# Kernel tuning notes

Measured on AMD Instinct MI355X. Metric: run time of the kernel, lower is better.

Reference implementation:

```python
import jax, jax.numpy as jnp
import numpy as np

D = 128      # memory_dim
L = 64       # segment_len
SCALE = 1.0 / np.sqrt(D)
LN_EPS = 1e-5


def _layernorm(x, g, b):
    mu = x.mean(-1, keepdims=True)
    var = ((x - mu) ** 2).mean(-1, keepdims=True)
    return (x - mu) * jax.lax.rsqrt(var + LN_EPS) * g + b


def setup_inputs() -> dict:
    key = jax.random.key(0)
    ks = jax.random.split(key, 8)
    B, T, Hd = 4, 4096, 2048
    w = 0.02  # init scale for weight matrices
    return {
        "H": jax.random.normal(ks[0], (B, T, Hd), jnp.float32),
        "M": jax.random.normal(ks[1], (B, D, D), jnp.float32),  # [B,K=128,D=128]
        "ln_g": jnp.ones((Hd,), jnp.float32),
        "ln_b": jnp.zeros((Hd,), jnp.float32),
        "W_eta_w": jax.random.normal(ks[2], (Hd,), jnp.float32) * w,
        "W_eta_b": jnp.full((1,), -5.0, jnp.float32),
        "sum_q": jax.random.normal(ks[3], (D,), jnp.float32),
        "sp_w": jax.random.normal(ks[4], (Hd, D), jnp.float32) * w,
        "sp_b": jnp.zeros((D,), jnp.float32),
        "eta_ch": jnp.ones((D,), jnp.float32),
        "temp": jnp.ones((1,), jnp.float32),
        "W_qkv": jax.random.normal(ks[5], (Hd, 3 * D), jnp.float32) * w,
    }


def reference(H, M, ln_g, ln_b, W_eta_w, W_eta_b, sum_q, sp_w, sp_b, eta_ch, temp, W_qkv):
    B, T, _ = H.shape
    K = M.shape[1]
    S = T // L  # T chosen divisible by segment_len (no-pad branch)

    Hn = _layernorm(H, ln_g, ln_b)                      # [B,T,Hd]

    # ---- write_memory ----
    H_mem = Hn @ sp_w + sp_b                            # [B,T,D]
    eta_tokens = jnp.einsum('bth,h->bt', Hn, W_eta_w) + W_eta_b  # [B,T]

    H_segs = H_mem.reshape(B, S, L, D)
    summary_scores = jnp.einsum('d,bsld->bsl', sum_q, H_segs) * SCALE
    summary_w = jax.nn.softmax(summary_scores, axis=-1)
    Z_seg = jnp.einsum('bsl,bsld->bsd', summary_w, H_segs)       # [B,S,D]

    eta_sig = jax.nn.sigmoid(eta_tokens)                          # [B,T]
    eta_seg = eta_sig.reshape(B, S, L).max(axis=-1)[..., None]    # [B,S,1]

    scores = jnp.einsum('bsd,bkd->bsk', Z_seg, M) * SCALE * jnp.exp(temp)
    A = jax.nn.softmax(scores, axis=-1)                           # [B,S,K]
    DeltaM = jnp.einsum('bsk,bsd->bkd', A, Z_seg * eta_seg)       # [B,K,D]

    eta_avg = eta_seg.mean(axis=1, keepdims=True)                 # [B,1,1]
    gate = eta_avg * jax.nn.sigmoid(eta_ch)                       # [B,1,D]
    M_new = (1.0 - gate) * M + DeltaM / S

    norm_sq = jnp.sum(DeltaM ** 2) / S
    # diversity loss on M_new
    Mn = M_new / jnp.maximum(jnp.linalg.norm(M_new, axis=-1, keepdims=True), 1e-12)
    sim = jnp.einsum('bkd,bjd->bkj', Mn, Mn) * (1.0 - jnp.eye(K, dtype=M.dtype))
    div_loss = jnp.mean(sim ** 2)
    loss = norm_sq * 0.01 + div_loss * 0.1

    # ---- read_memory (from updated memory; K<=1024 -> dense softmax path) ----
    Q_r = Hn @ W_qkv[:, 2 * D:]                                   # [B,T,D]
    r_scores = jnp.einsum('btd,bkd->btk', Q_r, M_new)
    A_r = jax.nn.softmax(r_scores * 2.0, axis=-1)
    C = jnp.einsum('btk,bkd->btd', A_r, M_new)                    # [B,T,D]

    return C, loss
```

## Files before the change

kernel.cpp:

```cpp
#include <hip/hip_runtime.h>
#include <hip/hip_bf16.h>
#include <math.h>

#define HD   2048
#define DD   128
#define TT   4096
#define BB   4
#define MT   (BB*TT)
#define LSEG 64
#define SSEG 64
#define NCOL 256
#define SCALE_D 0.088388347648318447f

typedef _Float16 half8 __attribute__((ext_vector_type(8)));
typedef _Float16 half4v __attribute__((ext_vector_type(4)));
typedef float    f32x4 __attribute__((ext_vector_type(4)));

__device__ __forceinline__ float sigmf(float x){ return 1.f/(1.f+__expf(-x)); }

__device__ __forceinline__ void glds16(const void* g, void* l) {
  __builtin_amdgcn_global_load_lds(
      (const __attribute__((address_space(1))) unsigned int*)g,
      (__attribute__((address_space(3))) unsigned int*)l, 16, 0, 0);
}

__global__ void k_pre(const float* __restrict__ ln_g, const float* __restrict__ ln_b,
                      const float* __restrict__ sp_w, const float* __restrict__ sp_b,
                      const float* __restrict__ W_qkv, const float* __restrict__ W_eta_w,
                      const float* __restrict__ W_eta_b,
                      _Float16* __restrict__ Bp, float* __restrict__ s_vec,
                      float* __restrict__ cb_vec, float* __restrict__ we2,
                      float* __restrict__ scal)
{
  __shared__ float red1[256], red2[256];
  int n = blockIdx.x, t = threadIdx.x;
  float sp = 0.f, cp = 0.f;
  if (n < NCOL) {
    for (int h = t; h < HD; h += 256) {
      float w = (n < DD) ? sp_w[(size_t)h*DD + n] : W_qkv[(size_t)h*384 + 256 + (n-DD)];
      float g = ln_g[h], b = ln_b[h];
      Bp[(size_t)n*HD + h] = (_Float16)(g*w);
      sp += g*w; cp += b*w;
    }
  } else {
    for (int h = t; h < HD; h += 256) {
      float w = W_eta_w[h];
      float g = ln_g[h], b = ln_b[h];
      we2[h] = g*w;
      sp += g*w; cp += b*w;
    }
  }
  red1[t] = sp; red2[t] = cp;
  __syncthreads();
  for (int o = 128; o > 0; o >>= 1) {
    if (t < o) { red1[t] += red1[t+o]; red2[t] += red2[t+o]; }
    __syncthreads();
  }
  if (t == 0) {
    if (n < NCOL) {
      s_vec[n]  = red1[0];
      cb_vec[n] = red2[0] + ((n < DD) ? sp_b[n] : 0.f);
    } else {
      scal[0] = red1[0];
      scal[1] = red2[0] + W_eta_b[0];
      scal[2] = 0.f; scal[3] = 0.f;
    }
  }
}

__launch_bounds__(512, 2)
__global__ void k01(const float* __restrict__ H, const _Float16* __restrict__ Bp,
                    const float* __restrict__ s_vec, const float* __restrict__ cb_vec,
                    const float* __restrict__ we2, const float* __restrict__ scal,
                    const float* __restrict__ sum_q, const float* __restrict__ Mmat,
                    const float* __restrict__ temp,
                    float* __restrict__ Q_r, float* __restrict__ Zeta,
                    float* __restrict__ A_seg, float* __restrict__ eta_seg)
{
  __shared__ __align__(16) char pool[114688];
  __shared__ float we_s[HD];
  __shared__ float smu[64], srs[64], seta[64];
  __shared__ float sq_s[128], w64_s[64], Zs[128], red_s[4];
  __shared__ float eta_sh_s;
  _Float16* sA  = (_Float16*)pool;
  _Float16* sB  = (_Float16*)(pool + 16384);
  float*    sHm = (float*)pool;

  int tid = threadIdx.x;
  int seg = blockIdx.x;
  int b   = seg >> 6;
  int m0  = seg * 64;
  int w = tid >> 6, lane = tid & 63;
  int wr = w >> 2, wc = w & 3;
  int fcol = lane & 15, kq = lane >> 4;

  for (int i = tid; i < HD/4; i += 512)
    ((float4*)we_s)[i] = ((const float4*)we2)[i];
  if (tid < 128) sq_s[tid] = sum_q[tid];
  float scal0 = scal[0], scal1 = scal[1];
  __syncthreads();

  int r_l = tid >> 3, s8 = tid & 7;
  const float* aptr = H + (size_t)(m0 + r_l)*HD + s8*8;
  int bn[4], bsl[4];
#pragma unroll
  for (int i = 0; i < 4; ++i) {
    int idx = i*512 + tid;
    bn[i]  = idx >> 3;
    bsl[i] = (idx & 7) ^ (bn[i] & 7);
  }

  f32x4 acc[2][4];
#pragma unroll
  for (int i = 0; i < 2; ++i)
#pragma unroll
    for (int j = 0; j < 4; ++j) acc[i][j] = (f32x4){0.f,0.f,0.f,0.f};
  float s1 = 0.f, s2 = 0.f, se = 0.f;

  float4 paE0 = *(const float4*)(aptr + 0);
  float4 paE1 = *(const float4*)(aptr + 4);
#pragma unroll
  for (int i = 0; i < 4; ++i)
    glds16(Bp + (size_t)bn[i]*HD + bsl[i]*8, sB + (size_t)(i*512 + tid)*8);
  float4 paO0 = *(const float4*)(aptr + 64);
  float4 paO1 = *(const float4*)(aptr + 68);
#pragma unroll
  for (int i = 0; i < 4; ++i)
    glds16(Bp + (size_t)bn[i]*HD + 64 + bsl[i]*8,
           sB + 16384 + (size_t)(i*512 + tid)*8);

  int cur3 = 0;

#define KSTEP(KT, P0, P1, VMASM, PREFETCH, BISSUE)                            \
  {                                                                           \
    _Float16* sAc = sA + ((KT)&1)*4096;                                       \
    _Float16* sBc = sB + cur3*16384;                                          \
    int k0 = (KT)*64;                                                         \
    float v[8] = {P0.x,P0.y,P0.z,P0.w, P1.x,P1.y,P1.z,P1.w};                  \
    if (PREFETCH) {                                                           \
      const float* ap_ = aptr + ((KT)+2)*64;                                  \
      P0 = *(const float4*)(ap_ + 0);                                         \
      P1 = *(const float4*)(ap_ + 4);                                         \
    }                                                                         \
    {                                                                         \
      const float4* wv4 = (const float4*)(we_s + k0 + s8*8);                  \
      float4 u0 = wv4[0], u1 = wv4[1];                                        \
      float uu[8] = {u0.x,u0.y,u0.z,u0.w, u1.x,u1.y,u1.z,u1.w};               \
      half8 h0;                                                               \
      _Pragma("unroll")                                                       \
      for (int j = 0; j < 8; ++j) {                                           \
        s1 += v[j]; s2 += v[j]*v[j]; se += v[j]*uu[j];                        \
        h0[j] = (_Float16)v[j];                                               \
      }                                                                       \
      *(half8*)&sAc[r_l*64 + (s8 ^ (r_l & 7))*8] = h0;                        \
    }                                                                         \
    asm volatile(VMASM ::: "memory");                                         \
    __builtin_amdgcn_s_barrier();                                             \
    __builtin_amdgcn_sched_barrier(0);                                        \
    if (BISSUE) {                                                             \
      int wb3 = cur3 + 2; if (wb3 >= 3) wb3 -= 3;                             \
      _Float16* sBn = sB + wb3*16384;                                         \
      const _Float16* bsrc = Bp + (k0 + 128);                                 \
      _Pragma("unroll")                                                       \
      for (int i = 0; i < 4; ++i)                                             \
        glds16(bsrc + (size_t)bn[i]*HD + bsl[i]*8,                            \
               sBn + (size_t)(i*512 + tid)*8);                                \
      __builtin_amdgcn_sched_barrier(0);                                      \
    }                                                                         \
    __builtin_amdgcn_s_setprio(1);                                            \
    _Pragma("unroll")                                                         \
    for (int ks = 0; ks < 2; ++ks) {                                          \
      half8 af[2], bf[4];                                                     \
      _Pragma("unroll")                                                       \
      for (int rt = 0; rt < 2; ++rt) {                                        \
        int r = wr*32 + rt*16 + fcol;                                         \
        int ch = (ks*4 + kq) ^ (r & 7);                                       \
        af[rt] = *(half8*)&sAc[r*64 + ch*8];                                  \
      }                                                                       \
      _Pragma("unroll")                                                       \
      for (int ct = 0; ct < 4; ++ct) {                                        \
        int n = wc*64 + ct*16 + fcol;                                         \
        int ch = (ks*4 + kq) ^ (n & 7);                                       \
        bf[ct] = *(half8*)&sBc[n*64 + ch*8];                                  \
      }                                                                       \
      _Pragma("unroll")                                                       \
      for (int rt = 0; rt < 2; ++rt)                                          \
        _Pragma("unroll")                                                     \
        for (int ct = 0; ct < 4; ++ct)                                        \
          acc[rt][ct] = __builtin_amdgcn_mfma_f32_16x16x32_f16(af[rt], bf[ct], acc[rt][ct], 0,0,0); \
    }                                                                         \
    __builtin_amdgcn_s_setprio(0);                                            \
    cur3 += 1; if (cur3 >= 3) cur3 -= 3;                                      \
  }

#pragma unroll 1
  for (int kp = 0; kp < 15; ++kp) {
    KSTEP(2*kp,   paE0, paE1, "s_waitcnt vmcnt(8) lgkmcnt(0)", 1, 1)
    KSTEP(2*kp+1, paO0, paO1, "s_waitcnt vmcnt(8) lgkmcnt(0)", 1, 1)
  }
  KSTEP(30, paE0, paE1, "s_waitcnt vmcnt(6) lgkmcnt(0)", 0, 0)
  KSTEP(31, paO0, paO1, "s_waitcnt vmcnt(0) lgkmcnt(0)", 0, 0)
#undef KSTEP

  s1 += __shfl_xor(s1, 1); s1 += __shfl_xor(s1, 2); s1 += __shfl_xor(s1, 4);
  s2 += __shfl_xor(s2, 1); s2 += __shfl_xor(s2, 2); s2 += __shfl_xor(s2, 4);
  se += __shfl_xor(se, 1); se += __shfl_xor(se, 2); se += __shfl_xor(se, 4);
  if (s8 == 0) {
    float mu   = s1 * (1.f/HD);
    float var  = s2 * (1.f/HD) - mu*mu;
    float rstd = rsqrtf(var + 1e-5f);
    smu[r_l] = mu; srs[r_l] = rstd;
    seta[r_l] = rstd*(se - mu*scal0) + scal1;
  }
  __syncthreads();

#pragma unroll
  for (int ct = 0; ct < 4; ++ct) {
    int nl = wc*64 + ct*16 + fcol;
    float sn = s_vec[nl], cbn = cb_vec[nl];
#pragma unroll
    for (int rt = 0; rt < 2; ++rt)
#pragma unroll
      for (int r = 0; r < 4; ++r) {
        int m = wr*32 + rt*16 + kq*4 + r;
        sHm[m*260 + nl] = srs[m]*(acc[rt][ct][r] - smu[m]*sn) + cbn;
      }
  }
  __syncthreads();

#pragma unroll
  for (int j = 0; j < 4; ++j) {
    int idx = j*512 + tid;
    int row = idx >> 5, c4 = (idx & 31)*4;
    *(float4*)&Q_r[(size_t)(m0 + row)*DD + c4] = *(float4*)&sHm[row*260 + 128 + c4];
  }

  if (w == 0) {
    float sc = 0.f;
    const float4* hrow = (const float4*)&sHm[lane*260];
#pragma unroll
    for (int d4 = 0; d4 < 32; ++d4) {
      float4 hv = hrow[d4];
      float4 qv = *(const float4*)&sq_s[d4*4];
      sc += hv.x*qv.x + hv.y*qv.y + hv.z*qv.z + hv.w*qv.w;
    }
    sc *= SCALE_D;
    float mx = sc;
    for (int o = 32; o > 0; o >>= 1) mx = fmaxf(mx, __shfl_xor(mx, o));
    float e = __expf(sc - mx);
    float sm = e;
    for (int o = 32; o > 0; o >>= 1) sm += __shfl_xor(sm, o);
    w64_s[lane] = e / sm;
  } else if (w == 1) {
    float ev = seta[lane];
    for (int o = 32; o > 0; o >>= 1) ev = fmaxf(ev, __shfl_xor(ev, o));
    if (lane == 0) { float es = sigmf(ev); eta_sh_s = es; eta_seg[seg] = es; }
  }
  __syncthreads();

  if (tid < 128) {
    float z = 0.f;
    for (int l = 0; l < 64; ++l) z += w64_s[l]*sHm[l*260 + tid];
    Zs[tid] = z;
    Zeta[(size_t)seg*DD + tid] = z * eta_sh_s;
  }
  __syncthreads();

  float sc2 = 0.f;
  if (tid < 128) {
    const float4* mrow = (const float4*)(Mmat + ((size_t)b*DD + tid)*DD);
#pragma unroll
    for (int d4 = 0; d4 < 32; ++d4) {
      float4 mv = mrow[d4];
      sc2 += mv.x*Zs[d4*4] + mv.y*Zs[d4*4+1] + mv.z*Zs[d4*4+2] + mv.w*Zs[d4*4+3];
    }
    sc2 *= SCALE_D * __expf(temp[0]);
    float mx = sc2;
    for (int o = 32; o > 0; o >>= 1) mx = fmaxf(mx, __shfl_xor(mx, o));
    if (lane == 0) red_s[w] = mx;
  }
  __syncthreads();
  float ev2 = 0.f;
  if (tid < 128) {
    float mx = fmaxf(red_s[0], red_s[1]);
    ev2 = __expf(sc2 - mx);
    float sm = ev2;
    for (int o = 32; o > 0; o >>= 1) sm += __shfl_xor(sm, o);
    if (lane == 0) red_s[2 + w] = sm;
  }
  __syncthreads();
  if (tid < 128) {
    float smt = red_s[2] + red_s[3];
    A_seg[(size_t)seg*DD + tid] = ev2 / smt;
  }
}

__global__ void k2b(const float* __restrict__ A_seg, const float* __restrict__ Zeta,
                    const float* __restrict__ eta_seg, const float* __restrict__ Mmat,
                    const float* __restrict__ eta_ch,
                    float* __restrict__ M_new, float* __restrict__ rns_arr,
                    float* __restrict__ scal)
{
  __shared__ float As[64][33];
  __shared__ __align__(16) float Zsl[64*128];
  __shared__ float rowp[32][8];
  __shared__ float eta_av;
  __shared__ float redb[4];
  int tid = threadIdx.x;
  int b = blockIdx.x >> 2, kq = blockIdx.x & 3;
  for (int i = tid; i < 64*32; i += 256) {
    int s = i >> 5, j = i & 31;
    As[s][j] = A_seg[((size_t)b*SSEG + s)*DD + kq*32 + j];
  }
  const float4* z4 = (const float4*)(Zeta + (size_t)b*SSEG*DD);
  float4* zs4 = (float4*)Zsl;
  for (int i = tid; i < 64*32; i += 256) zs4[i] = z4[i];
  if (tid < 64) {
    float ev = eta_seg[(size_t)b*SSEG + tid];
    for (int o=32;o>0;o>>=1) ev += __shfl_xor(ev, o);
    if (tid == 0) eta_av = ev * (1.f/SSEG);
  }
  __syncthreads();
  int kl = tid & 31, dg = tid >> 5;
  int k = kq*32 + kl, d0 = dg*16;
  float dm[16];
#pragma unroll
  for (int j=0;j<16;j++) dm[j]=0.f;
  for (int s = 0; s < 64; ++s) {
    float a = As[s][kl];
    const float* zr = &Zsl[s*128 + d0];
#pragma unroll
    for (int j=0;j<16;j++) dm[j] += a * zr[j];
  }
  float nsq = 0.f;
#pragma unroll
  for (int j=0;j<16;j++) nsq += dm[j]*dm[j];
  float eav = eta_av;
  float mn[16];
  float ss = 0.f;
#pragma unroll
  for (int j=0;j<16;j++) {
    int d = d0 + j;
    float gate = eav * sigmf(eta_ch[d]);
    float v = (1.f - gate)*Mmat[((size_t)b*DD + k)*DD + d] + dm[j]*(1.f/SSEG);
    mn[j] = v; ss += v*v;
  }
#pragma unroll
  for (int j=0;j<16;j+=4) {
    float4 v4; v4.x=mn[j]; v4.y=mn[j+1]; v4.z=mn[j+2]; v4.w=mn[j+3];
    *(float4*)&M_new[((size_t)b*DD + k)*DD + d0 + j] = v4;
  }
  rowp[kl][dg] = ss;
  for (int o=1;o<64;o<<=1) nsq += __shfl_xor(nsq, o);
  if ((tid&63)==0) redb[tid>>6] = nsq;
  __syncthreads();
  if (tid == 0) atomicAdd(&scal[2], redb[0]+redb[1]+redb[2]+redb[3]);
  if (tid < 32) {
    float t2 = 0.f;
#pragma unroll
    for (int g=0; g<8; ++g) t2 += rowp[tid][g];
    float nrm = sqrtf(t2);
    rns_arr[(size_t)b*DD + kq*32 + tid] = 1.f / fmaxf(nrm, 1e-12f);
  }
}

__global__ void k2d(const float* __restrict__ M_new, const float* __restrict__ rns_arr,
                    float* __restrict__ scal)
{
  __shared__ float kr[4][128];
  __shared__ float redb[4];
  int tid = threadIdx.x;
  int b = blockIdx.x >> 5, kq = blockIdx.x & 31;
  for (int i = tid; i < 4*128; i += 256) {
    int ki = i >> 7, d = i & 127;
    kr[ki][d] = M_new[((size_t)b*DD + kq*4 + ki)*DD + d];
  }
  __syncthreads();
  int j = tid & 127, kh = tid >> 7;
  const float* mj = &M_new[((size_t)b*DD + j)*DD];
  float rj = rns_arr[(size_t)b*DD + j];
  float dv = 0.f;
#pragma unroll
  for (int ki2 = 0; ki2 < 2; ++ki2) {
    int kil = kh*2 + ki2;
    int kk = kq*4 + kil;
    float dot = 0.f;
    for (int d = 0; d < 128; d += 4) {
      float4 a = *(const float4*)(mj + d);
      dot += a.x*kr[kil][d] + a.y*kr[kil][d+1] + a.z*kr[kil][d+2] + a.w*kr[kil][d+3];
    }
    if (kk != j) {
      float sv = dot * rj * rns_arr[(size_t)b*DD + kk];
      dv += sv*sv;
    }
  }
  for (int o=1;o<64;o<<=1) dv += __shfl_xor(dv, o);
  if ((tid&63)==0) redb[tid>>6] = dv;
  __syncthreads();
  if (tid==0) atomicAdd(&scal[3], redb[0]+redb[1]+redb[2]+redb[3]);
}

__launch_bounds__(256, 1)
__global__ void k3(const float* __restrict__ Q_r, const float* __restrict__ M_new,
                   const float* __restrict__ scal, float* __restrict__ out)
{
  __shared__ __align__(16) _Float16 Mq[128*132];
  __shared__ __align__(16) _Float16 Mt[128*136];
  __shared__ __align__(16) _Float16 Ps[64*132];
  int tid = threadIdx.x;
  int b = blockIdx.x >> 6, tile = blockIdx.x & 63;
  int t0 = tile*64;
  if (blockIdx.x == 0 && tid == 0) {
    float loss = 0.01f*(scal[2]*(1.f/SSEG)) + 0.1f*(scal[3]*(1.f/(BB*DD*DD)));
    out[(size_t)MT*DD] = loss;
  }
  const float4* m4 = (const float4*)(M_new + (size_t)b*DD*DD);
#pragma unroll
  for (int it = 0; it < 4; ++it) {
    int sb = it*256 + tid;
    int rb = sb & 31, cb = sb >> 5;
    int r0 = rb*4, c0 = cb*4;
    float a[4][4];
#pragma unroll
    for (int j = 0; j < 4; ++j) {
      float4 v = m4[(size_t)(r0+j)*32 + cb];
      a[j][0]=v.x; a[j][1]=v.y; a[j][2]=v.z; a[j][3]=v.w;
    }
#pragma unroll
    for (int j = 0; j < 4; ++j) {
      half4v h; h.x=(_Float16)a[j][0]; h.y=(_Float16)a[j][1];
                h.z=(_Float16)a[j][2]; h.w=(_Float16)a[j][3];
      *(half4v*)&Mq[(r0+j)*132 + c0] = h;
    }
#pragma unroll
    for (int j2 = 0; j2 < 4; ++j2) {
      half4v h; h.x=(_Float16)a[0][j2]; h.y=(_Float16)a[1][j2];
                h.z=(_Float16)a[2][j2]; h.w=(_Float16)a[3][j2];
      *(half4v*)&Mt[(c0+j2)*136 + r0] = h;
    }
  }
  int w = tid >> 6, lane = tid & 63;
  int fcol = lane & 15, kq = lane >> 4;
  int tokA = t0 + w*16 + fcol;
  size_t qbase = ((size_t)b*TT + tokA)*DD;
  half8 af[4];
#pragma unroll
  for (int ks = 0; ks < 4; ++ks) {
    float4 q0 = *(const float4*)&Q_r[qbase + ks*32 + kq*8];
    float4 q1 = *(const float4*)&Q_r[qbase + ks*32 + kq*8 + 4];
    half8 h;
    h[0]=(_Float16)q0.x; h[1]=(_Float16)q0.y; h[2]=(_Float16)q0.z; h[3]=(_Float16)q0.w;
    h[4]=(_Float16)q1.x; h[5]=(_Float16)q1.y; h[6]=(_Float16)q1.z; h[7]=(_Float16)q1.w;
    af[ks] = h;
  }
  __syncthreads();
  f32x4 sacc[8];
#pragma unroll
  for (int nt = 0; nt < 8; ++nt) sacc[nt] = (f32x4){0.f,0.f,0.f,0.f};
#pragma unroll
  for (int nt = 0; nt < 8; ++nt)
#pragma unroll
    for (int ks = 0; ks < 4; ++ks) {
      half8 bf = *(half8*)&Mq[(nt*16 + fcol)*132 + ks*32 + kq*8];
      sacc[nt] = __builtin_amdgcn_mfma_f32_16x16x32_f16(af[ks], bf, sacc[nt], 0,0,0);
    }
#pragma unroll
  for (int nt = 0; nt < 8; ++nt)
#pragma unroll
    for (int r = 0; r < 4; ++r) sacc[nt][r] *= 2.f;
  float mx[4], sm[4];
#pragma unroll
  for (int r = 0; r < 4; ++r) {
    float m = sacc[0][r];
#pragma unroll
    for (int nt = 1; nt < 8; ++nt) m = fmaxf(m, sacc[nt][r]);
#pragma unroll
    for (int o = 1; o < 16; o <<= 1) m = fmaxf(m, __shfl_xor(m, o));
    mx[r] = m;
  }
#pragma unroll
  for (int r = 0; r < 4; ++r) sm[r] = 0.f;
#pragma unroll
  for (int nt = 0; nt < 8; ++nt)
#pragma unroll
    for (int r = 0; r < 4; ++r) {
      float e = __expf(sacc[nt][r] - mx[r]);
      sacc[nt][r] = e; sm[r] += e;
    }
#pragma unroll
  for (int r = 0; r < 4; ++r) {
    float s = sm[r];
#pragma unroll
    for (int o = 1; o < 16; o <<= 1) s += __shfl_xor(s, o);
    sm[r] = 1.f / s;
  }
#pragma unroll
  for (int nt = 0; nt < 8; ++nt)
#pragma unroll
    for (int r = 0; r < 4; ++r) {
      int tk = w*16 + kq*4 + r;
      Ps[tk*132 + nt*16 + fcol] = (_Float16)(sacc[nt][r]*sm[r]);
    }
  __syncthreads();
  half8 pf[4];
#pragma unroll
  for (int ks = 0; ks < 4; ++ks)
    pf[ks] = *(half8*)&Ps[(w*16 + fcol)*132 + ks*32 + kq*8];
  f32x4 cacc[8];
#pragma unroll
  for (int nt = 0; nt < 8; ++nt) cacc[nt] = (f32x4){0.f,0.f,0.f,0.f};
#pragma unroll
  for (int nt = 0; nt < 8; ++nt)
#pragma unroll
    for (int ks = 0; ks < 4; ++ks) {
      half8 bf = *(half8*)&Mt[(nt*16 + fcol)*136 + ks*32 + kq*8];
      cacc[nt] = __builtin_amdgcn_mfma_f32_16x16x32_f16(pf[ks], bf, cacc[nt], 0,0,0);
    }
#pragma unroll
  for (int nt = 0; nt < 8; ++nt)
#pragma unroll
    for (int r = 0; r < 4; ++r) {
      int tk = t0 + w*16 + kq*4 + r;
      out[((size_t)b*TT + tk)*DD + nt*16 + fcol] = cacc[nt][r];
    }
}

extern "C" void kernel_launch(void* const* d_in, const int* in_sizes, int n_in,
                              void* d_out, int out_size, void* d_ws, size_t ws_size,
                              hipStream_t stream)
{
  (void)in_sizes; (void)n_in; (void)out_size; (void)ws_size;
  const float* H       = (const float*)d_in[0];
  const float* Mmat    = (const float*)d_in[1];
  const float* ln_g    = (const float*)d_in[2];
  const float* ln_b    = (const float*)d_in[3];
  const float* W_eta_w = (const float*)d_in[4];
  const float* W_eta_b = (const float*)d_in[5];
  const float* sum_q   = (const float*)d_in[6];
  const float* sp_w    = (const float*)d_in[7];
  const float* sp_b    = (const float*)d_in[8];
  const float* eta_ch  = (const float*)d_in[9];
  const float* temp    = (const float*)d_in[10];
  const float* W_qkv   = (const float*)d_in[11];
  float* out           = (float*)d_out;

  char* wsb = (char*)d_ws;
  size_t off = 0;
  auto alloc = [&](size_t bytes) -> void* {
    void* p = wsb + off;
    off = (off + bytes + 255) & ~(size_t)255;
    return p;
  };
  _Float16* Bp   = (_Float16*)alloc((size_t)NCOL*HD*2);
  float* s_vec   = (float*)alloc(NCOL*4);
  float* cb_vec  = (float*)alloc(NCOL*4);
  float* we2     = (float*)alloc(HD*4);
  float* scal    = (float*)alloc(4*4);
  float* Q_r     = (float*)alloc((size_t)MT*DD*4);
  float* Zeta    = (float*)alloc((size_t)BB*SSEG*DD*4);
  float* A_seg   = (float*)alloc((size_t)BB*SSEG*DD*4);
  float* eta_seg = (float*)alloc((size_t)BB*SSEG*4);
  float* M_new   = (float*)alloc((size_t)BB*DD*DD*4);
  float* rns_arr = (float*)alloc((size_t)BB*DD*4);

  hipLaunchKernelGGL(k_pre, dim3(NCOL+1), dim3(256), 0, stream,
                     ln_g, ln_b, sp_w, sp_b, W_qkv, W_eta_w, W_eta_b,
                     Bp, s_vec, cb_vec, we2, scal);
  hipLaunchKernelGGL(k01, dim3(MT/64), dim3(512), 0, stream,
                     H, Bp, s_vec, cb_vec, we2, scal, sum_q, Mmat, temp,
                     Q_r, Zeta, A_seg, eta_seg);
  hipLaunchKernelGGL(k2b, dim3(16), dim3(256), 0, stream,
                     A_seg, Zeta, eta_seg, Mmat, eta_ch, M_new, rns_arr, scal);
  hipLaunchKernelGGL(k2d, dim3(128), dim3(256), 0, stream,
                     M_new, rns_arr, scal);
  hipLaunchKernelGGL(k3, dim3(256), dim3(256), 0, stream,
                     Q_r, M_new, scal, out);
}
```

Baseline: 87.06 us.

## Deepen k01 GEMM pipeline to four B stages and four-step A prefetch

Changes the fused layernorm+GEMM kernel's main loop from a 3-stage LDS ring for B with 2-step-ahead register prefetch of H to a 4-stage B ring with 4-step-ahead H prefetch. The loop is unrolled by four with static buffer indices, and the vmcnt waits are retuned. The goal is to hide more global-memory latency on the H stream and the weight tiles. In exchange it uses more LDS (pool grows to 144KB) and more registers, which may reduce occupancy below the 2 blocks per CU the launch bounds target.

```diff
diff --git a/kernel.cpp b/kernel.cpp
--- a/kernel.cpp
+++ b/kernel.cpp
@@ -77,7 +77,7 @@
                     float* __restrict__ Q_r, float* __restrict__ Zeta,
                     float* __restrict__ A_seg, float* __restrict__ eta_seg)
 {
-  __shared__ __align__(16) char pool[114688];
+  __shared__ __align__(16) char pool[147456];
   __shared__ float we_s[HD];
   __shared__ float smu[64], srs[64], seta[64];
   __shared__ float sq_s[128], w64_s[64], Zs[128], red_s[4];
@@ -117,32 +117,35 @@
     for (int j = 0; j < 4; ++j) acc[i][j] = (f32x4){0.f,0.f,0.f,0.f};
   float s1 = 0.f, s2 = 0.f, se = 0.f;
 
-  float4 paE0 = *(const float4*)(aptr + 0);
-  float4 paE1 = *(const float4*)(aptr + 4);
+  float4 q0a = *(const float4*)(aptr + 0),   q0b = *(const float4*)(aptr + 4);
+  float4 q1a = *(const float4*)(aptr + 64),  q1b = *(const float4*)(aptr + 68);
+  __builtin_amdgcn_sched_barrier(0);
 #pragma unroll
   for (int i = 0; i < 4; ++i)
     glds16(Bp + (size_t)bn[i]*HD + bsl[i]*8, sB + (size_t)(i*512 + tid)*8);
-  float4 paO0 = *(const float4*)(aptr + 64);
-  float4 paO1 = *(const float4*)(aptr + 68);
+  __builtin_amdgcn_sched_barrier(0);
+  float4 q2a = *(const float4*)(aptr + 128), q2b = *(const float4*)(aptr + 132);
+  __builtin_amdgcn_sched_barrier(0);
 #pragma unroll
   for (int i = 0; i < 4; ++i)
     glds16(Bp + (size_t)bn[i]*HD + 64 + bsl[i]*8,
            sB + 16384 + (size_t)(i*512 + tid)*8);
-
-  int cur3 = 0;
-
-#define KSTEP(KT, P0, P1, VMASM, PREFETCH, BISSUE)                            \
+  __builtin_amdgcn_sched_barrier(0);
+  float4 q3a = *(const float4*)(aptr + 192), q3b = *(const float4*)(aptr + 196);
+  __builtin_amdgcn_sched_barrier(0);
+#pragma unroll
+  for (int i = 0; i < 4; ++i)
+    glds16(Bp + (size_t)bn[i]*HD + 128 + bsl[i]*8,
+           sB + 32768 + (size_t)(i*512 + tid)*8);
+  __builtin_amdgcn_sched_barrier(0);
+
+#define KSTEP(K0V, SAB, SBBUF, SBNB, P0, P1, VMASM, APREF, BISSUE)            \
   {                                                                           \
-    _Float16* sAc = sA + ((KT)&1)*4096;                                       \
-    _Float16* sBc = sB + cur3*16384;                                          \
-    int k0 = (KT)*64;                                                         \
-    float v[8] = {P0.x,P0.y,P0.z,P0.w, P1.x,P1.y,P1.z,P1.w};                  \
-    if (PREFETCH) {                                                           \
-      const float* ap_ = aptr + ((KT)+2)*64;                                  \
-      P0 = *(const float4*)(ap_ + 0);                                         \
-      P1 = *(const float4*)(ap_ + 4);                                         \
-    }                                                                         \
+    _Float16* sAc = sA + (SAB)*4096;                                          \
+    _Float16* sBc = sB + (SBBUF)*16384;                                       \
+    const int k0 = (K0V);                                                     \
     {                                                                         \
+      float v[8] = {P0.x,P0.y,P0.z,P0.w, P1.x,P1.y,P1.z,P1.w};                \
       const float4* wv4 = (const float4*)(we_s + k0 + s8*8);                  \
       float4 u0 = wv4[0], u1 = wv4[1];                                        \
       float uu[8] = {u0.x,u0.y,u0.z,u0.w, u1.x,u1.y,u1.z,u1.w};               \
@@ -158,13 +161,18 @@
     __builtin_amdgcn_s_barrier();                                             \
     __builtin_amdgcn_sched_barrier(0);                                        \
     if (BISSUE) {                                                             \
-      int wb3 = cur3 + 2; if (wb3 >= 3) wb3 -= 3;                             \
-      _Float16* sBn = sB + wb3*16384;                                         \
-      const _Float16* bsrc = Bp + (k0 + 128);                                 \
+      _Float16* sBn = sB + (SBNB)*16384;                                      \
+      const _Float16* bsrc = Bp + (k0 + 192);                                 \
       _Pragma("unroll")                                                       \
       for (int i = 0; i < 4; ++i)                                             \
         glds16(bsrc + (size_t)bn[i]*HD + bsl[i]*8,                            \
                sBn + (size_t)(i*512 + tid)*8);                                \
+      __builtin_amdgcn_sched_barrier(0);                                      \
+    }                                                                         \
+    if (APREF) {                                                              \
+      const float* ap_ = aptr + k0 + 256;                                     \
+      P0 = *(const float4*)(ap_ + 0);                                         \
+      P1 = *(const float4*)(ap_ + 4);                                         \
       __builtin_amdgcn_sched_barrier(0);                                      \
     }                                                                         \
     __builtin_amdgcn_s_setprio(1);                                            \
@@ -190,16 +198,24 @@
           acc[rt][ct] = __builtin_amdgcn_mfma_f32_16x16x32_f16(af[rt], bf[ct], acc[rt][ct], 0,0,0); \
     }                                                                         \
     __builtin_amdgcn_s_setprio(0);                                            \
-    cur3 += 1; if (cur3 >= 3) cur3 -= 3;                                      \
-  }
-
+  }
+
+  KSTEP(0,   0, 0, 3, q0a, q0b, "s_waitcnt vmcnt(12) lgkmcnt(0)", 1, 1)
+  KSTEP(64,  1, 1, 0, q1a, q1b, "s_waitcnt vmcnt(12) lgkmcnt(0)", 1, 1)
+  KSTEP(128, 0, 2, 1, q2a, q2b, "s_waitcnt vmcnt(12) lgkmcnt(0)", 1, 1)
+  KSTEP(192, 1, 3, 2, q3a, q3b, "s_waitcnt vmcnt(14) lgkmcnt(0)", 1, 1)
 #pragma unroll 1
-  for (int kp = 0; kp < 15; ++kp) {
-    KSTEP(2*kp,   paE0, paE1, "s_waitcnt vmcnt(8) lgkmcnt(0)", 1, 1)
-    KSTEP(2*kp+1, paO0, paO1, "s_waitcnt vmcnt(8) lgkmcnt(0)", 1, 1)
-  }
-  KSTEP(30, paE0, paE1, "s_waitcnt vmcnt(6) lgkmcnt(0)", 0, 0)
-  KSTEP(31, paO0, paO1, "s_waitcnt vmcnt(0) lgkmcnt(0)", 0, 0)
+  for (int kp = 1; kp < 7; ++kp) {
+    int j0 = kp*256;
+    KSTEP(j0,     0, 0, 3, q0a, q0b, "s_waitcnt vmcnt(14) lgkmcnt(0)", 1, 1)
+    KSTEP(j0+64,  1, 1, 0, q1a, q1b, "s_waitcnt vmcnt(14) lgkmcnt(0)", 1, 1)
+    KSTEP(j0+128, 0, 2, 1, q2a, q2b, "s_waitcnt vmcnt(14) lgkmcnt(0)", 1, 1)
+    KSTEP(j0+192, 1, 3, 2, q3a, q3b, "s_waitcnt vmcnt(14) lgkmcnt(0)", 1, 1)
+  }
+  KSTEP(1792, 0, 0, 3, q0a, q0b, "s_waitcnt vmcnt(14) lgkmcnt(0)", 0, 1)
+  KSTEP(1856, 1, 1, 0, q1a, q1b, "s_waitcnt vmcnt(12) lgkmcnt(0)", 0, 0)
+  KSTEP(1920, 0, 2, 1, q2a, q2b, "s_waitcnt vmcnt(6) lgkmcnt(0)",  0, 0)
+  KSTEP(1984, 1, 3, 2, q3a, q3b, "s_waitcnt vmcnt(0) lgkmcnt(0)",  0, 0)
 #undef KSTEP
 
   s1 += __shfl_xor(s1, 1); s1 += __shfl_xor(s1, 2); s1 += __shfl_xor(s1, 4);
```

New measurement: 89.00 us. 1.02x slower.

## Halve K-tile of fused LN-GEMM kernel to fit four blocks per CU

Applied to the files above, without the earlier changes.

Shrinks the fused LayerNorm+projection kernel's K-step from 64 to 32 and cuts the LDS pool from about 114KB to 65KB, moving we_s into the pool. Launch bounds rise to 4 blocks per SM so more waves can hide the H loads and the B-panel global_load_lds traffic. The pipeline gets a new swizzle and tuned waitcnt values, and the loop now runs 64 steps with twice as many barriers. sHm epilogue reuse of the smaller pool (64 rows by 260 floats is about 66.5KB) must still fit, and the register cap tightens.

```diff
diff --git a/kernel.cpp b/kernel.cpp
--- a/kernel.cpp
+++ b/kernel.cpp
@@ -68,7 +68,7 @@
   }
 }
 
-__launch_bounds__(512, 2)
+__launch_bounds__(512, 4)
 __global__ void k01(const float* __restrict__ H, const _Float16* __restrict__ Bp,
                     const float* __restrict__ s_vec, const float* __restrict__ cb_vec,
                     const float* __restrict__ we2, const float* __restrict__ scal,
@@ -77,14 +77,14 @@
                     float* __restrict__ Q_r, float* __restrict__ Zeta,
                     float* __restrict__ A_seg, float* __restrict__ eta_seg)
 {
-  __shared__ __align__(16) char pool[114688];
-  __shared__ float we_s[HD];
+  __shared__ __align__(16) char pool[66560];
   __shared__ float smu[64], srs[64], seta[64];
   __shared__ float sq_s[128], w64_s[64], Zs[128], red_s[4];
   __shared__ float eta_sh_s;
-  _Float16* sA  = (_Float16*)pool;
-  _Float16* sB  = (_Float16*)(pool + 16384);
-  float*    sHm = (float*)pool;
+  _Float16* sA   = (_Float16*)pool;
+  _Float16* sB   = (_Float16*)(pool + 8192);
+  float*    we_s = (float*)(pool + 57344);
+  float*    sHm  = (float*)pool;
 
   int tid = threadIdx.x;
   int seg = blockIdx.x;
@@ -94,20 +94,18 @@
   int wr = w >> 2, wc = w & 3;
   int fcol = lane & 15, kq = lane >> 4;
 
-  for (int i = tid; i < HD/4; i += 512)
-    ((float4*)we_s)[i] = ((const float4*)we2)[i];
+  ((float4*)we_s)[tid] = ((const float4*)we2)[tid];
   if (tid < 128) sq_s[tid] = sum_q[tid];
-  float scal0 = scal[0], scal1 = scal[1];
-  __syncthreads();
-
-  int r_l = tid >> 3, s8 = tid & 7;
-  const float* aptr = H + (size_t)(m0 + r_l)*HD + s8*8;
-  int bn[4], bsl[4];
-#pragma unroll
-  for (int i = 0; i < 4; ++i) {
+  __syncthreads();
+
+  int r_l = tid >> 3, s4 = tid & 7;
+  const float* aptr = H + (size_t)(m0 + r_l)*HD + s4*4;
+  int bn[2], bsl[2];
+#pragma unroll
+  for (int i = 0; i < 2; ++i) {
     int idx = i*512 + tid;
-    bn[i]  = idx >> 3;
-    bsl[i] = (idx & 7) ^ (bn[i] & 7);
+    bn[i]  = idx >> 2;
+    bsl[i] = (idx & 3) ^ ((bn[i] >> 1) & 3);
   }
 
   f32x4 acc[2][4];
@@ -117,71 +115,61 @@
     for (int j = 0; j < 4; ++j) acc[i][j] = (f32x4){0.f,0.f,0.f,0.f};
   float s1 = 0.f, s2 = 0.f, se = 0.f;
 
-  float4 paE0 = *(const float4*)(aptr + 0);
-  float4 paE1 = *(const float4*)(aptr + 4);
-#pragma unroll
-  for (int i = 0; i < 4; ++i)
-    glds16(Bp + (size_t)bn[i]*HD + bsl[i]*8, sB + (size_t)(i*512 + tid)*8);
-  float4 paO0 = *(const float4*)(aptr + 64);
-  float4 paO1 = *(const float4*)(aptr + 68);
-#pragma unroll
-  for (int i = 0; i < 4; ++i)
-    glds16(Bp + (size_t)bn[i]*HD + 64 + bsl[i]*8,
-           sB + 16384 + (size_t)(i*512 + tid)*8);
+  float4 paE = *(const float4*)(aptr);
+  __builtin_amdgcn_sched_barrier(0);
+  glds16(Bp + (size_t)bn[0]*HD + bsl[0]*8, sB + (size_t)tid*8);
+  glds16(Bp + (size_t)bn[1]*HD + bsl[1]*8, sB + (size_t)(512 + tid)*8);
+  __builtin_amdgcn_sched_barrier(0);
+  float4 paO = *(const float4*)(aptr + 32);
+  __builtin_amdgcn_sched_barrier(0);
+  glds16(Bp + (size_t)bn[0]*HD + 32 + bsl[0]*8, sB + 8192 + (size_t)tid*8);
+  glds16(Bp + (size_t)bn[1]*HD + 32 + bsl[1]*8, sB + 8192 + (size_t)(512 + tid)*8);
+  __builtin_amdgcn_sched_barrier(0);
 
   int cur3 = 0;
 
-#define KSTEP(KT, P0, P1, VMASM, PREFETCH, BISSUE)                            \
+#define KSTEP(K0V, SAB, P, VMASM, APREF, BISSUE)                              \
   {                                                                           \
-    _Float16* sAc = sA + ((KT)&1)*4096;                                       \
-    _Float16* sBc = sB + cur3*16384;                                          \
-    int k0 = (KT)*64;                                                         \
-    float v[8] = {P0.x,P0.y,P0.z,P0.w, P1.x,P1.y,P1.z,P1.w};                  \
-    if (PREFETCH) {                                                           \
-      const float* ap_ = aptr + ((KT)+2)*64;                                  \
-      P0 = *(const float4*)(ap_ + 0);                                         \
-      P1 = *(const float4*)(ap_ + 4);                                         \
-    }                                                                         \
+    _Float16* sAc = sA + (SAB)*2048;                                          \
+    _Float16* sBc = sB + cur3*8192;                                           \
+    const int k0 = (K0V);                                                     \
     {                                                                         \
-      const float4* wv4 = (const float4*)(we_s + k0 + s8*8);                  \
-      float4 u0 = wv4[0], u1 = wv4[1];                                        \
-      float uu[8] = {u0.x,u0.y,u0.z,u0.w, u1.x,u1.y,u1.z,u1.w};               \
-      half8 h0;                                                               \
-      _Pragma("unroll")                                                       \
-      for (int j = 0; j < 8; ++j) {                                           \
-        s1 += v[j]; s2 += v[j]*v[j]; se += v[j]*uu[j];                        \
-        h0[j] = (_Float16)v[j];                                               \
-      }                                                                       \
-      *(half8*)&sAc[r_l*64 + (s8 ^ (r_l & 7))*8] = h0;                        \
+      float v0 = P.x, v1 = P.y, v2 = P.z, v3 = P.w;                           \
+      const float4 u = *(const float4*)(we_s + k0 + s4*4);                    \
+      s1 += (v0+v1)+(v2+v3);                                                  \
+      s2 += (v0*v0+v1*v1)+(v2*v2+v3*v3);                                      \
+      se += (v0*u.x+v1*u.y)+(v2*u.z+v3*u.w);                                  \
+      half4v h; h.x=(_Float16)v0; h.y=(_Float16)v1;                           \
+                h.z=(_Float16)v2; h.w=(_Float16)v3;                           \
+      *(half4v*)&sAc[r_l*32 + (((s4>>1)^((r_l>>1)&3))<<3) + ((s4&1)<<2)] = h; \
     }                                                                         \
     asm volatile(VMASM ::: "memory");                                         \
     __builtin_amdgcn_s_barrier();                                             \
     __builtin_amdgcn_sched_barrier(0);                                        \
     if (BISSUE) {                                                             \
       int wb3 = cur3 + 2; if (wb3 >= 3) wb3 -= 3;                             \
-      _Float16* sBn = sB + wb3*16384;                                         \
-      const _Float16* bsrc = Bp + (k0 + 128);                                 \
-      _Pragma("unroll")                                                       \
-      for (int i = 0; i < 4; ++i)                                             \
-        glds16(bsrc + (size_t)bn[i]*HD + bsl[i]*8,                            \
-               sBn + (size_t)(i*512 + tid)*8);                                \
+      _Float16* sBn = sB + wb3*8192;                                          \
+      const _Float16* bsrc = Bp + (k0 + 64);                                  \
+      glds16(bsrc + (size_t)bn[0]*HD + bsl[0]*8, sBn + (size_t)tid*8);        \
+      glds16(bsrc + (size_t)bn[1]*HD + bsl[1]*8, sBn + (size_t)(512+tid)*8);  \
+      __builtin_amdgcn_sched_barrier(0);                                      \
+    }                                                                         \
+    if (APREF) {                                                              \
+      P = *(const float4*)(aptr + k0 + 64);                                   \
       __builtin_amdgcn_sched_barrier(0);                                      \
     }                                                                         \
     __builtin_amdgcn_s_setprio(1);                                            \
-    _Pragma("unroll")                                                         \
-    for (int ks = 0; ks < 2; ++ks) {                                          \
+    {                                                                         \
       half8 af[2], bf[4];                                                     \
       _Pragma("unroll")                                                       \
       for (int rt = 0; rt < 2; ++rt) {                                        \
         int r = wr*32 + rt*16 + fcol;                                         \
-        int ch = (ks*4 + kq) ^ (r & 7);                                       \
-        af[rt] = *(half8*)&sAc[r*64 + ch*8];                                  \
+        af[rt] = *(half8*)&sAc[r*32 + ((kq ^ ((r>>1)&3))<<3)];                \
       }                                                                       \
       _Pragma("unroll")                                                       \
       for (int ct = 0; ct < 4; ++ct) {                                        \
         int n = wc*64 + ct*16 + fcol;                                         \
-        int ch = (ks*4 + kq) ^ (n & 7);                                       \
-        bf[ct] = *(half8*)&sBc[n*64 + ch*8];                                  \
+        bf[ct] = *(half8*)&sBc[n*32 + ((kq ^ ((n>>1)&3))<<3)];                \
       }                                                                       \
       _Pragma("unroll")                                                       \
       for (int rt = 0; rt < 2; ++rt)                                          \
@@ -194,18 +182,20 @@
   }
 
 #pragma unroll 1
-  for (int kp = 0; kp < 15; ++kp) {
-    KSTEP(2*kp,   paE0, paE1, "s_waitcnt vmcnt(8) lgkmcnt(0)", 1, 1)
-    KSTEP(2*kp+1, paO0, paO1, "s_waitcnt vmcnt(8) lgkmcnt(0)", 1, 1)
-  }
-  KSTEP(30, paE0, paE1, "s_waitcnt vmcnt(6) lgkmcnt(0)", 0, 0)
-  KSTEP(31, paO0, paO1, "s_waitcnt vmcnt(0) lgkmcnt(0)", 0, 0)
+  for (int kp = 0; kp < 31; ++kp) {
+    int j0 = kp*64;
+    KSTEP(j0,      0, paE, "s_waitcnt vmcnt(3) lgkmcnt(0)", 1, 1)
+    KSTEP(j0 + 32, 1, paO, "s_waitcnt vmcnt(3) lgkmcnt(0)", 1, 1)
+  }
+  KSTEP(1984, 0, paE, "s_waitcnt vmcnt(3) lgkmcnt(0)", 0, 0)
+  KSTEP(2016, 1, paO, "s_waitcnt vmcnt(0) lgkmcnt(0)", 0, 0)
 #undef KSTEP
 
   s1 += __shfl_xor(s1, 1); s1 += __shfl_xor(s1, 2); s1 += __shfl_xor(s1, 4);
   s2 += __shfl_xor(s2, 1); s2 += __shfl_xor(s2, 2); s2 += __shfl_xor(s2, 4);
   se += __shfl_xor(se, 1); se += __shfl_xor(se, 2); se += __shfl_xor(se, 4);
-  if (s8 == 0) {
+  float scal0 = scal[0], scal1 = scal[1];
+  if (s4 == 0) {
     float mu   = s1 * (1.f/HD);
     float var  = s2 * (1.f/HD) - mu*mu;
     float rstd = rsqrtf(var + 1e-5f);
```

New measurement: 107.8 us. 1.24x slower.

## Load H A-fragments directly into registers, dropping the LDS staging for A

Applied to the files above, without the earlier changes.

Each wave now loads the fp32 H rows it needs for its MFMA A-fragments straight from global memory into registers and converts them to fp16 in place. This removes the LDS A buffer, its writes and reads, and shrinks shared memory. The layernorm and eta statistics are computed only by two waves that between them cover all rows, and the loop is unrolled so the triple B buffer indices are compile-time constants. The cost is that every wave re-reads overlapping H rows from global memory (each row is loaded by four waves), and register pressure rises from holding sixteen float4 prefetch values.

```diff
diff --git a/kernel.cpp b/kernel.cpp
--- a/kernel.cpp
+++ b/kernel.cpp
@@ -22,6 +22,20 @@
   __builtin_amdgcn_global_load_lds(
       (const __attribute__((address_space(1))) unsigned int*)g,
       (__attribute__((address_space(3))) unsigned int*)l, 16, 0, 0);
+}
+
+__device__ __forceinline__ half8 cvt8(float4 a, float4 b) {
+  half8 h;
+  h[0]=(_Float16)a.x; h[1]=(_Float16)a.y; h[2]=(_Float16)a.z; h[3]=(_Float16)a.w;
+  h[4]=(_Float16)b.x; h[5]=(_Float16)b.y; h[6]=(_Float16)b.z; h[7]=(_Float16)b.w;
+  return h;
+}
+
+__device__ __forceinline__ void acc3(float4 v, float4 u,
+                                     float& s1, float& s2, float& se) {
+  s1 += (v.x+v.y)+(v.z+v.w);
+  s2 += (v.x*v.x+v.y*v.y)+(v.z*v.z+v.w*v.w);
+  se += (v.x*u.x+v.y*u.y)+(v.z*u.z+v.w*u.w);
 }
 
 __global__ void k_pre(const float* __restrict__ ln_g, const float* __restrict__ ln_b,
@@ -77,13 +91,12 @@
                     float* __restrict__ Q_r, float* __restrict__ Zeta,
                     float* __restrict__ A_seg, float* __restrict__ eta_seg)
 {
-  __shared__ __align__(16) char pool[114688];
+  __shared__ __align__(16) char pool[98304];
   __shared__ float we_s[HD];
   __shared__ float smu[64], srs[64], seta[64];
   __shared__ float sq_s[128], w64_s[64], Zs[128], red_s[4];
   __shared__ float eta_sh_s;
-  _Float16* sA  = (_Float16*)pool;
-  _Float16* sB  = (_Float16*)(pool + 16384);
+  _Float16* sB  = (_Float16*)pool;
   float*    sHm = (float*)pool;
 
   int tid = threadIdx.x;
@@ -93,6 +106,7 @@
   int w = tid >> 6, lane = tid & 63;
   int wr = w >> 2, wc = w & 3;
   int fcol = lane & 15, kq = lane >> 4;
+  bool SW = (w == 0) || (w == 7);
 
   for (int i = tid; i < HD/4; i += 512)
     ((float4*)we_s)[i] = ((const float4*)we2)[i];
@@ -100,8 +114,9 @@
   float scal0 = scal[0], scal1 = scal[1];
   __syncthreads();
 
-  int r_l = tid >> 3, s8 = tid & 7;
-  const float* aptr = H + (size_t)(m0 + r_l)*HD + s8*8;
+  int ra = m0 + wr*32 + fcol, rb = ra + 16;
+  const float* aA = H + (size_t)ra*HD + kq*8;
+  const float* aB = H + (size_t)rb*HD + kq*8;
   int bn[4], bsl[4];
 #pragma unroll
   for (int i = 0; i < 4; ++i) {
@@ -115,51 +130,55 @@
   for (int i = 0; i < 2; ++i)
 #pragma unroll
     for (int j = 0; j < 4; ++j) acc[i][j] = (f32x4){0.f,0.f,0.f,0.f};
-  float s1 = 0.f, s2 = 0.f, se = 0.f;
-
-  float4 paE0 = *(const float4*)(aptr + 0);
-  float4 paE1 = *(const float4*)(aptr + 4);
+  float s1a=0.f,s2a=0.f,sea=0.f, s1b=0.f,s2b=0.f,seb=0.f;
+
+  float4 E0,E1,E2,E3,E4,E5,E6,E7, O0,O1,O2,O3,O4,O5,O6,O7;
+  E0=*(const float4*)(aA+0);  E1=*(const float4*)(aA+4);
+  E2=*(const float4*)(aA+32); E3=*(const float4*)(aA+36);
+  E4=*(const float4*)(aB+0);  E5=*(const float4*)(aB+4);
+  E6=*(const float4*)(aB+32); E7=*(const float4*)(aB+36);
+  __builtin_amdgcn_sched_barrier(0);
 #pragma unroll
   for (int i = 0; i < 4; ++i)
     glds16(Bp + (size_t)bn[i]*HD + bsl[i]*8, sB + (size_t)(i*512 + tid)*8);
-  float4 paO0 = *(const float4*)(aptr + 64);
-  float4 paO1 = *(const float4*)(aptr + 68);
+  __builtin_amdgcn_sched_barrier(0);
+  O0=*(const float4*)(aA+64); O1=*(const float4*)(aA+68);
+  O2=*(const float4*)(aA+96); O3=*(const float4*)(aA+100);
+  O4=*(const float4*)(aB+64); O5=*(const float4*)(aB+68);
+  O6=*(const float4*)(aB+96); O7=*(const float4*)(aB+100);
+  __builtin_amdgcn_sched_barrier(0);
 #pragma unroll
   for (int i = 0; i < 4; ++i)
     glds16(Bp + (size_t)bn[i]*HD + 64 + bsl[i]*8,
            sB + 16384 + (size_t)(i*512 + tid)*8);
-
-  int cur3 = 0;
-
-#define KSTEP(KT, P0, P1, VMASM, PREFETCH, BISSUE)                            \
+  __builtin_amdgcn_sched_barrier(0);
+
+#define KSTEP(K0V, CUR, WB, P0,P1,P2,P3,P4,P5,P6,P7, VMASM, ISSUE)            \
   {                                                                           \
-    _Float16* sAc = sA + ((KT)&1)*4096;                                       \
-    _Float16* sBc = sB + cur3*16384;                                          \
-    int k0 = (KT)*64;                                                         \
-    float v[8] = {P0.x,P0.y,P0.z,P0.w, P1.x,P1.y,P1.z,P1.w};                  \
-    if (PREFETCH) {                                                           \
-      const float* ap_ = aptr + ((KT)+2)*64;                                  \
-      P0 = *(const float4*)(ap_ + 0);                                         \
-      P1 = *(const float4*)(ap_ + 4);                                         \
+    _Float16* sBc = sB + (CUR)*16384;                                         \
+    const int k0 = (K0V);                                                     \
+    if (SW) {                                                                 \
+      float4 u0 = *(const float4*)(we_s + k0 + kq*8);                         \
+      float4 u1 = *(const float4*)(we_s + k0 + kq*8 + 4);                     \
+      float4 u2 = *(const float4*)(we_s + k0 + 32 + kq*8);                    \
+      float4 u3 = *(const float4*)(we_s + k0 + 32 + kq*8 + 4);                \
+      acc3(P0,u0,s1a,s2a,sea); acc3(P1,u1,s1a,s2a,sea);                       \
+      acc3(P2,u2,s1a,s2a,sea); acc3(P3,u3,s1a,s2a,sea);                       \
+      acc3(P4,u0,s1b,s2b,seb); acc3(P5,u1,s1b,s2b,seb);                       \
+      acc3(P6,u2,s1b,s2b,seb); acc3(P7,u3,s1b,s2b,seb);                       \
     }                                                                         \
-    {                                                                         \
-      const float4* wv4 = (const float4*)(we_s + k0 + s8*8);                  \
-      float4 u0 = wv4[0], u1 = wv4[1];                                        \
-      float uu[8] = {u0.x,u0.y,u0.z,u0.w, u1.x,u1.y,u1.z,u1.w};               \
-      half8 h0;                                                               \
-      _Pragma("unroll")                                                       \
-      for (int j = 0; j < 8; ++j) {                                           \
-        s1 += v[j]; s2 += v[j]*v[j]; se += v[j]*uu[j];                        \
-        h0[j] = (_Float16)v[j];                                               \
-      }                                                                       \
-      *(half8*)&sAc[r_l*64 + (s8 ^ (r_l & 7))*8] = h0;                        \
-    }                                                                         \
+    half8 afA0 = cvt8(P0,P1), afA1 = cvt8(P2,P3);                             \
+    half8 afB0 = cvt8(P4,P5), afB1 = cvt8(P6,P7);                             \
     asm volatile(VMASM ::: "memory");                                         \
     __builtin_amdgcn_s_barrier();                                             \
     __builtin_amdgcn_sched_barrier(0);                                        \
-    if (BISSUE) {                                                             \
-      int wb3 = cur3 + 2; if (wb3 >= 3) wb3 -= 3;                             \
-      _Float16* sBn = sB + wb3*16384;                                         \
+    if (ISSUE) {                                                              \
+      P0=*(const float4*)(aA+k0+128); P1=*(const float4*)(aA+k0+132);         \
+      P2=*(const float4*)(aA+k0+160); P3=*(const float4*)(aA+k0+164);         \
+      P4=*(const float4*)(aB+k0+128); P5=*(const float4*)(aB+k0+132);         \
+      P6=*(const float4*)(aB+k0+160); P7=*(const float4*)(aB+k0+164);         \
+      __builtin_amdgcn_sched_barrier(0);                                      \
+      _Float16* sBn = sB + (WB)*16384;                                        \
       const _Float16* bsrc = Bp + (k0 + 128);                                 \
       _Pragma("unroll")                                                       \
       for (int i = 0; i < 4; ++i)                                             \
@@ -170,47 +189,58 @@
     __builtin_amdgcn_s_setprio(1);                                            \
     _Pragma("unroll")                                                         \
     for (int ks = 0; ks < 2; ++ks) {                                          \
-      half8 af[2], bf[4];                                                     \
-      _Pragma("unroll")                                                       \
-      for (int rt = 0; rt < 2; ++rt) {                                        \
-        int r = wr*32 + rt*16 + fcol;                                         \
-        int ch = (ks*4 + kq) ^ (r & 7);                                       \
-        af[rt] = *(half8*)&sAc[r*64 + ch*8];                                  \
-      }                                                                       \
+      half8 bf[4];                                                            \
       _Pragma("unroll")                                                       \
       for (int ct = 0; ct < 4; ++ct) {                                        \
         int n = wc*64 + ct*16 + fcol;                                         \
         int ch = (ks*4 + kq) ^ (n & 7);                                       \
         bf[ct] = *(half8*)&sBc[n*64 + ch*8];                                  \
       }                                                                       \
+      half8 a0 = ks ? afA1 : afA0;                                            \
+      half8 a1 = ks ? afB1 : afB0;                                            \
       _Pragma("unroll")                                                       \
-      for (int rt = 0; rt < 2; ++rt)                                          \
-        _Pragma("unroll")                                                     \
-        for (int ct = 0; ct < 4; ++ct)                                        \
-          acc[rt][ct] = __builtin_amdgcn_mfma_f32_16x16x32_f16(af[rt], bf[ct], acc[rt][ct], 0,0,0); \
+      for (int ct = 0; ct < 4; ++ct) {                                        \
+        acc[0][ct] = __builtin_amdgcn_mfma_f32_16x16x32_f16(a0, bf[ct], acc[0][ct], 0,0,0); \
+        acc[1][ct] = __builtin_amdgcn_mfma_f32_16x16x32_f16(a1, bf[ct], acc[1][ct], 0,0,0); \
+      }                                                                       \
     }                                                                         \
     __builtin_amdgcn_s_setprio(0);                                            \
-    cur3 += 1; if (cur3 >= 3) cur3 -= 3;                                      \
   }
 
 #pragma unroll 1
-  for (int kp = 0; kp < 15; ++kp) {
-    KSTEP(2*kp,   paE0, paE1, "s_waitcnt vmcnt(8) lgkmcnt(0)", 1, 1)
-    KSTEP(2*kp+1, paO0, paO1, "s_waitcnt vmcnt(8) lgkmcnt(0)", 1, 1)
-  }
-  KSTEP(30, paE0, paE1, "s_waitcnt vmcnt(6) lgkmcnt(0)", 0, 0)
-  KSTEP(31, paO0, paO1, "s_waitcnt vmcnt(0) lgkmcnt(0)", 0, 0)
+  for (int kp = 0; kp < 5; ++kp) {
+    int j0 = kp*384;
+    KSTEP(j0,       0, 2, E0,E1,E2,E3,E4,E5,E6,E7, "s_waitcnt vmcnt(12)", 1)
+    KSTEP(j0 + 64,  1, 0, O0,O1,O2,O3,O4,O5,O6,O7, "s_waitcnt vmcnt(12)", 1)
+    KSTEP(j0 + 128, 2, 1, E0,E1,E2,E3,E4,E5,E6,E7, "s_waitcnt vmcnt(12)", 1)
+    KSTEP(j0 + 192, 0, 2, O0,O1,O2,O3,O4,O5,O6,O7, "s_waitcnt vmcnt(12)", 1)
+    KSTEP(j0 + 256, 1, 0, E0,E1,E2,E3,E4,E5,E6,E7, "s_waitcnt vmcnt(12)", 1)
+    KSTEP(j0 + 320, 2, 1, O0,O1,O2,O3,O4,O5,O6,O7, "s_waitcnt vmcnt(12)", 1)
+  }
+  KSTEP(1920, 0, 2, E0,E1,E2,E3,E4,E5,E6,E7, "s_waitcnt vmcnt(12)", 0)
+  KSTEP(1984, 1, 0, O0,O1,O2,O3,O4,O5,O6,O7, "s_waitcnt vmcnt(0)",  0)
 #undef KSTEP
 
-  s1 += __shfl_xor(s1, 1); s1 += __shfl_xor(s1, 2); s1 += __shfl_xor(s1, 4);
-  s2 += __shfl_xor(s2, 1); s2 += __shfl_xor(s2, 2); s2 += __shfl_xor(s2, 4);
-  se += __shfl_xor(se, 1); se += __shfl_xor(se, 2); se += __shfl_xor(se, 4);
-  if (s8 == 0) {
-    float mu   = s1 * (1.f/HD);
-    float var  = s2 * (1.f/HD) - mu*mu;
-    float rstd = rsqrtf(var + 1e-5f);
-    smu[r_l] = mu; srs[r_l] = rstd;
-    seta[r_l] = rstd*(se - mu*scal0) + scal1;
+  if (SW) {
+    s1a += __shfl_xor(s1a,16); s1a += __shfl_xor(s1a,32);
+    s2a += __shfl_xor(s2a,16); s2a += __shfl_xor(s2a,32);
+    sea += __shfl_xor(sea,16); sea += __shfl_xor(sea,32);
+    s1b += __shfl_xor(s1b,16); s1b += __shfl_xor(s1b,32);
+    s2b += __shfl_xor(s2b,16); s2b += __shfl_xor(s2b,32);
+    seb += __shfl_xor(seb,16); seb += __shfl_xor(seb,32);
+    if (kq == 0) {
+      int base = wr*32;
+      float mua   = s1a*(1.f/HD);
+      float vara  = s2a*(1.f/HD) - mua*mua;
+      float rsa   = rsqrtf(vara + 1e-5f);
+      smu[base+fcol] = mua; srs[base+fcol] = rsa;
+      seta[base+fcol] = rsa*(sea - mua*scal0) + scal1;
+      float mub   = s1b*(1.f/HD);
+      float varb  = s2b*(1.f/HD) - mub*mub;
+      float rsb   = rsqrtf(varb + 1e-5f);
+      smu[base+16+fcol] = mub; srs[base+16+fcol] = rsb;
+      seta[base+16+fcol] = rsb*(seb - mub*scal0) + scal1;
+    }
   }
   __syncthreads();
 
```

After: 130.6 us. +50.0%, slower.
